# Optimization experiments

Hardware: AMD Instinct MI355X
Metric: run time of the kernel (lower is better)

## Reference

```python
import jax, jax.numpy as jnp
import numpy as np

B, S, D, H = 2, 2048, 1024, 16
DH = D // H  # 64


def setup_inputs() -> dict:
    key = jax.random.key(0)
    ks = jax.random.split(key, 12)
    scale = 0.02
    q = jax.random.normal(ks[0], (B, S, D), dtype=jnp.float32)
    k = jax.random.normal(ks[1], (B, S, D), dtype=jnp.float32)
    v = jax.random.normal(ks[2], (B, S, D), dtype=jnp.float32)
    # CTRL-style causal mask: 1.0 above the diagonal (positions to mask), 0.0 elsewhere
    mask = jnp.triu(jnp.ones((S, S), dtype=jnp.float32), k=1)
    Wq = jax.random.normal(ks[3], (D, D), dtype=jnp.float32) * scale
    bq = jnp.zeros((D,), dtype=jnp.float32)
    Wk = jax.random.normal(ks[4], (D, D), dtype=jnp.float32) * scale
    bk = jnp.zeros((D,), dtype=jnp.float32)
    Wv = jax.random.normal(ks[5], (D, D), dtype=jnp.float32) * scale
    bv = jnp.zeros((D,), dtype=jnp.float32)
    Wo = jax.random.normal(ks[6], (D, D), dtype=jnp.float32) * scale
    bo = jnp.zeros((D,), dtype=jnp.float32)
    return {"q": q, "k": k, "v": v, "mask": mask,
            "Wq": Wq, "bq": bq, "Wk": Wk, "bk": bk,
            "Wv": Wv, "bv": bv, "Wo": Wo, "bo": bo}


def _split_heads(x):
    # [B, S, D] -> [B, H, S, DH]
    b, s, _ = x.shape
    return x.reshape(b, s, H, DH).transpose(0, 2, 1, 3)


def reference(q, k, v, mask, Wq, bq, Wk, bk, Wv, bv, Wo, bo):
    # QKV projections
    qh = _split_heads(q @ Wq + bq)  # [B, H, S, DH]
    kh = _split_heads(k @ Wk + bk)
    vh = _split_heads(v @ Wv + bv)
    # scaled dot-product attention with CTRL mask convention (mask * -1e4 added)
    scores = jnp.einsum('bhqd,bhkd->bhqk', qh, kh) / jnp.sqrt(jnp.float32(DH))
    scores = scores + mask * -10000.0  # mask broadcasts [S,S] -> [B,H,S,S]
    weights = jax.nn.softmax(scores, axis=-1)
    ctx = jnp.einsum('bhqk,bhkd->bhqd', weights, vh)  # [B, H, S, DH]
    ctx = ctx.transpose(0, 2, 1, 3).reshape(q.shape[0], -1, D)  # [B, S, D]
    return ctx @ Wo + bo
```

## Files before the change

kernel.cpp:

```cpp
#include <hip/hip_runtime.h>
#include <stdint.h>

typedef unsigned short u16;
typedef __attribute__((ext_vector_type(8))) short bf16x8;
typedef __attribute__((ext_vector_type(4))) float f32x4;
typedef __attribute__((ext_vector_type(4))) unsigned short u16x4;

#define C_SCALE 0.1803368801111204f
#define C_MASK  -14426.950408889634f

__device__ __forceinline__ float bf2f(u16 x) {
  union { uint32_t u; float f; } v; v.u = ((uint32_t)x) << 16; return v.f;
}
__device__ __forceinline__ u16 f2bf(float f) {
  union { float f; uint32_t u; } v; v.f = f;
  return (u16)((v.u + 0x7FFFu + ((v.u >> 16) & 1u)) >> 16);
}

__device__ __forceinline__ void load_lds16(const void* g, void* l) {
  __builtin_amdgcn_global_load_lds(
      (const __attribute__((address_space(1))) uint32_t*)g,
      (__attribute__((address_space(3))) uint32_t*)l, 16, 0, 0);
}

__device__ __forceinline__ uint32_t pack_trunc(uint32_t f_even, uint32_t f_odd) {
  return __builtin_amdgcn_perm(f_odd, f_even, 0x07060302u);
}

union U4B { uint4 u; bf16x8 v; };

__global__ __launch_bounds__(256) void detect_dtype(const u16* __restrict__ q,
                                                    uint32_t* __restrict__ flag) {
  const int tid = threadIdx.x;
  u16 w = q[tid];
  int e = (w >> 7) & 0xFF;
  int ok = (e >= 96 && e <= 159) ? 1 : 0;
  unsigned long long b = __ballot(ok);
  __shared__ int cnt[4];
  if ((tid & 63) == 0) cnt[tid >> 6] = __popcll(b);
  __syncthreads();
  if (tid == 0) {
    int total = cnt[0] + cnt[1] + cnt[2] + cnt[3];
    *flag = (total >= 220) ? 1u : 0u;
  }
}

__global__ __launch_bounds__(256) void transpose_all(const u16* __restrict__ W0,
                                                     const u16* __restrict__ W1,
                                                     const u16* __restrict__ W2,
                                                     const u16* __restrict__ W3,
                                                     u16* __restrict__ WTb,
                                                     const uint32_t* __restrict__ flag) {
  constexpr int D = 1024;
  __shared__ u16 tile[64][72];
  const int z = blockIdx.z;
  const u16* W = z == 0 ? W0 : (z == 1 ? W1 : (z == 2 ? W2 : W3));
  u16* WT = WTb + (size_t)z * D * D;
  const bool isbf = (*flag != 0);
  const int x0 = blockIdx.x * 64, y0 = blockIdx.y * 64;
  const int t = threadIdx.x;
  const int r = t >> 3;
  const int c8 = (t & 7) << 3;
#pragma unroll
  for (int hh = 0; hh < 2; ++hh) {
    int row = r + hh * 32;
    if (isbf) {
      *(uint4*)&tile[row][c8] = *(const uint4*)&W[(size_t)(y0 + row) * D + x0 + c8];
    } else {
      const float* Wf = (const float*)W;
      float4 f0 = *(const float4*)&Wf[(size_t)(y0 + row) * D + x0 + c8];
      float4 f1 = *(const float4*)&Wf[(size_t)(y0 + row) * D + x0 + c8 + 4];
      u16 tmp[8] = {f2bf(f0.x), f2bf(f0.y), f2bf(f0.z), f2bf(f0.w),
                    f2bf(f1.x), f2bf(f1.y), f2bf(f1.z), f2bf(f1.w)};
      *(uint4*)&tile[row][c8] = *(uint4*)tmp;
    }
  }
  __syncthreads();
#pragma unroll
  for (int hh = 0; hh < 2; ++hh) {
    int row = r + hh * 32;
    u16 tmp[8];
#pragma unroll
    for (int i = 0; i < 8; ++i) tmp[i] = tile[c8 + i][row];
    *(uint4*)&WT[(size_t)(x0 + row) * D + y0 + c8] = *(uint4*)tmp;
  }
}

__global__ __launch_bounds__(256, 2) void gemm_qkv(
    const u16* __restrict__ A0, const u16* __restrict__ A1, const u16* __restrict__ A2,
    const u16* __restrict__ WTb,
    const u16* __restrict__ b0, const u16* __restrict__ b1, const u16* __restrict__ b2,
    u16* __restrict__ Chb, const uint32_t* __restrict__ flag) {
  constexpr int K = 1024;
  __shared__ u16 As[2][128 * 64];
  __shared__ u16 Bs[2][128 * 32];
  const int z = blockIdx.z;
  const u16* A = z == 0 ? A0 : (z == 1 ? A1 : A2);
  const u16* bias = z == 0 ? b0 : (z == 1 ? b1 : b2);
  const u16* BT = WTb + (size_t)z * 1024 * 1024;
  u16* C = Chb + (size_t)z * 4 * 1024 * 1024;
  const bool isbf = (*flag != 0);
  const int tid = threadIdx.x;
  const int wave = tid >> 6, lane = tid & 63;
  const int quad = lane >> 4, lr = lane & 15;
  const int f = blockIdx.x + 8 * blockIdx.y;
  const int n0 = (f >> 5) * 128;
  const int m0 = (f & 31) * 128;
  const int mW = (wave & 1) * 64, nW = (wave >> 1) * 64;

  auto stageB = [&](int k0, int kb) {
#pragma unroll
    for (int p = 0; p < 2; ++p) {
      int s = (wave * 2 + p) * 64 + lane;
      int r = s >> 2, c = s & 3;
      load_lds16(&BT[(size_t)(n0 + r) * K + k0 + c * 8], &Bs[kb][(wave * 2 + p) * 512]);
    }
  };

  f32x4 acc[4][4] = {};

  if (!isbf) {
    const uint32_t* Af = (const uint32_t*)A;
    auto stageA = [&](int k0, int kb) {
#pragma unroll
      for (int p = 0; p < 4; ++p) {
        int s = (wave * 4 + p) * 64 + lane;
        int r = s >> 3, cg = (s & 7) ^ (r & 7);
        load_lds16(&Af[(size_t)(m0 + r) * K + k0 + cg * 4],
                   &As[kb][(wave * 4 + p) * 512]);
      }
    };
    stageA(0, 0); stageB(0, 0);
    int kb = 0;
    for (int k0 = 0; k0 < K; k0 += 32, kb ^= 1) {
      __syncthreads();
      if (k0 + 32 < K) { stageA(k0 + 32, kb ^ 1); stageB(k0 + 32, kb ^ 1); }
      const uint32_t* As32 = (const uint32_t*)&As[kb][0];
      bf16x8 af[4], bfm[4];
#pragma unroll
      for (int i = 0; i < 4; ++i) {
        int r = mW + 16 * i + lr;
        int s0 = (2 * quad) ^ (r & 7), s1 = (2 * quad + 1) ^ (r & 7);
        uint4 lo = *(const uint4*)&As32[r * 32 + s0 * 4];
        uint4 hi = *(const uint4*)&As32[r * 32 + s1 * 4];
        U4B pk;
        pk.u.x = pack_trunc(lo.x, lo.y); pk.u.y = pack_trunc(lo.z, lo.w);
        pk.u.z = pack_trunc(hi.x, hi.y); pk.u.w = pack_trunc(hi.z, hi.w);
        af[i] = pk.v;
        bfm[i] = *(const bf16x8*)&Bs[kb][(nW + 16 * i + lr) * 32 + quad * 8];
      }
#pragma unroll
      for (int i = 0; i < 4; ++i)
#pragma unroll
        for (int j = 0; j < 4; ++j)
          acc[i][j] =
              __builtin_amdgcn_mfma_f32_16x16x32_bf16(af[i], bfm[j], acc[i][j], 0, 0, 0);
    }
  } else {
    auto stageAb = [&](int k0, int kb) {
#pragma unroll
      for (int p = 0; p < 2; ++p) {
        int s = (wave * 2 + p) * 64 + lane;
        int r = s >> 2, c = s & 3;
        load_lds16(&A[(size_t)(m0 + r) * K + k0 + c * 8], &As[kb][(wave * 2 + p) * 512]);
      }
    };
    stageAb(0, 0); stageB(0, 0);
    int kb = 0;
    for (int k0 = 0; k0 < K; k0 += 32, kb ^= 1) {
      __syncthreads();
      if (k0 + 32 < K) { stageAb(k0 + 32, kb ^ 1); stageB(k0 + 32, kb ^ 1); }
      bf16x8 af[4], bfm[4];
#pragma unroll
      for (int i = 0; i < 4; ++i) {
        af[i]  = *(const bf16x8*)&As[kb][(mW + 16 * i + lr) * 32 + quad * 8];
        bfm[i] = *(const bf16x8*)&Bs[kb][(nW + 16 * i + lr) * 32 + quad * 8];
      }
#pragma unroll
      for (int i = 0; i < 4; ++i)
#pragma unroll
        for (int j = 0; j < 4; ++j)
          acc[i][j] =
              __builtin_amdgcn_mfma_f32_16x16x32_bf16(af[i], bfm[j], acc[i][j], 0, 0, 0);
    }
  }

#pragma unroll
  for (int i = 0; i < 4; ++i) {
#pragma unroll
    for (int j = 0; j < 4; ++j) {
      int n = n0 + nW + 16 * j + lr;
      float bv = isbf ? bf2f(bias[n]) : ((const float*)bias)[n];
#pragma unroll
      for (int r = 0; r < 4; ++r) {
        int m = m0 + mW + 16 * i + quad * 4 + r;
        float val = acc[i][j][r] + bv;
        int b = m >> 11, s = m & 2047, h = n >> 6, dh = n & 63;
        C[((size_t)(b * 16 + h) * 2048 + s) * 64 + dh] = f2bf(val);
      }
    }
  }
}

__global__ __launch_bounds__(256, 2) void gemm_out(const u16* __restrict__ A,
                                                   const u16* __restrict__ BT,
                                                   const u16* __restrict__ bias,
                                                   u16* __restrict__ C,
                                                   const uint32_t* __restrict__ flag) {
  constexpr int K = 1024, N = 1024;
  __shared__ u16 As[2][64 * 32];
  __shared__ u16 Bs[2][128 * 32];
  const bool isbf = (*flag != 0);
  const int tid = threadIdx.x;
  const int wave = tid >> 6, lane = tid & 63;
  const int quad = lane >> 4, lr = lane & 15;
  const int f = blockIdx.x + 8 * blockIdx.y;
  const int n0 = (f >> 6) * 128;
  const int m0 = (f & 63) * 64;
  const int mW = (wave & 1) * 32, nW = (wave >> 1) * 64;

  auto stage = [&](int k0, int kb) {
    {
      int s = wave * 64 + lane;
      int r = s >> 2, c = s & 3;
      load_lds16(&A[(size_t)(m0 + r) * K + k0 + c * 8], &As[kb][wave * 512]);
    }
#pragma unroll
    for (int p = 0; p < 2; ++p) {
      int s = (wave * 2 + p) * 64 + lane;
      int r = s >> 2, c = s & 3;
      load_lds16(&BT[(size_t)(n0 + r) * K + k0 + c * 8], &Bs[kb][(wave * 2 + p) * 512]);
    }
  };

  f32x4 acc[2][4] = {};
  stage(0, 0);
  int kb = 0;
  for (int k0 = 0; k0 < K; k0 += 32, kb ^= 1) {
    __syncthreads();
    if (k0 + 32 < K) stage(k0 + 32, kb ^ 1);
    bf16x8 af[2], bfm[4];
#pragma unroll
    for (int i = 0; i < 2; ++i)
      af[i] = *(const bf16x8*)&As[kb][(mW + 16 * i + lr) * 32 + quad * 8];
#pragma unroll
    for (int j = 0; j < 4; ++j)
      bfm[j] = *(const bf16x8*)&Bs[kb][(nW + 16 * j + lr) * 32 + quad * 8];
#pragma unroll
    for (int i = 0; i < 2; ++i)
#pragma unroll
      for (int j = 0; j < 4; ++j)
        acc[i][j] =
            __builtin_amdgcn_mfma_f32_16x16x32_bf16(af[i], bfm[j], acc[i][j], 0, 0, 0);
  }

#pragma unroll
  for (int i = 0; i < 2; ++i) {
#pragma unroll
    for (int j = 0; j < 4; ++j) {
      int n = n0 + nW + 16 * j + lr;
      float bv = isbf ? bf2f(bias[n]) : ((const float*)bias)[n];
#pragma unroll
      for (int r = 0; r < 4; ++r) {
        int m = m0 + mW + 16 * i + quad * 4 + r;
        float val = acc[i][j][r] + bv;
        size_t idx = (size_t)m * N + n;
        if (isbf) C[idx] = f2bf(val);
        else ((float*)C)[idx] = val;
      }
    }
  }
}

__global__ __launch_bounds__(256, 2) void attn_fwd(const u16* __restrict__ Qh,
                                                   const u16* __restrict__ Kh,
                                                   const u16* __restrict__ Vh,
                                                   u16* __restrict__ ctx) {
  constexpr int S = 2048, DH = 64, Dm = 1024;
  __shared__ u16 Ks[2][64 * 64];
  __shared__ u16 Vt[64 * 72];
  __shared__ u16 Pl[4][16 * 72];
  const int tid = threadIdx.x;
  const int wave = tid >> 6, lane = tid & 63;
  const int quad = lane >> 4, lr = lane & 15;
  const int bh = blockIdx.y;
  const int bx = (int)blockIdx.x;
  const size_t base = (size_t)bh * S * DH;
  const u16* Q = Qh + base;
  const u16* Kp = Kh + base;
  const u16* Vp = Vh + base;
  u16* Plw = Pl[wave];
  const int b = bh >> 4, h = bh & 15;

  const int vkey2 = (tid & 31) * 2, vd8 = (tid >> 5) * 8;
  uint4 va, vb;

  auto stageK = [&](int kt, int kb) {
#pragma unroll
    for (int p = 0; p < 2; ++p) {
      int s = (wave * 2 + p) * 64 + lane;
      int r = s >> 3, cg = (s & 7) ^ (r & 7);
      load_lds16(&Kp[(size_t)(kt + r) * DH + cg * 8], &Ks[kb][(wave * 2 + p) * 512]);
    }
  };
  auto loadV = [&](int kt) {
    va = *(const uint4*)&Vp[(size_t)(kt + vkey2) * DH + vd8];
    vb = *(const uint4*)&Vp[(size_t)(kt + vkey2 + 1) * DH + vd8];
  };
  auto writeV = [&]() {
    const u16* pa = (const u16*)&va;
    const u16* pb = (const u16*)&vb;
#pragma unroll
    for (int i = 0; i < 8; ++i) {
      uint32_t pair = (uint32_t)pa[i] | ((uint32_t)pb[i] << 16);
      *(uint32_t*)&Vt[(vd8 + i) * 72 + vkey2] = pair;
    }
  };

  int kb = 0;
  for (int ph = 0; ph < 2; ++ph) {
    const int qt = ph == 0 ? (31 - bx) : bx;
    const int q0 = qt * 64;
    const int nt = qt + 1;
    const int qg = q0 + wave * 16 + lr;

    bf16x8 aQ[2];
#pragma unroll
    for (int s = 0; s < 2; ++s)
      aQ[s] = *(const bf16x8*)&Q[(size_t)(q0 + wave * 16 + lr) * DH + s * 32 + quad * 8];

    f32x4 o[4] = {};
    float m_i = -1.0e5f;
    float l_i = 0.f;

    __syncthreads();
    stageK(0, kb);
    loadV(0);

    for (int it = 0; it < nt; ++it) {
      const int kt = it * 64;
      __syncthreads();
      writeV();
      __syncthreads();

      bf16x8 aK[4][2], bV[4][2];
#pragma unroll
      for (int t = 0; t < 4; ++t) {
        int r = t * 16 + lr;
#pragma unroll
        for (int s = 0; s < 2; ++s) {
          int ch = (s * 4 + quad) ^ (r & 7);
          aK[t][s] = *(const bf16x8*)&Ks[kb][r * 64 + ch * 8];
        }
      }
#pragma unroll
      for (int c = 0; c < 4; ++c)
#pragma unroll
        for (int s = 0; s < 2; ++s)
          bV[c][s] = *(const bf16x8*)&Vt[(c * 16 + lr) * 72 + s * 32 + quad * 8];

      if (it + 1 < nt) { stageK(kt + 64, kb ^ 1); loadV(kt + 64); }

      f32x4 sc[4];
#pragma unroll
      for (int t = 0; t < 4; ++t) {
        f32x4 zz = {0.f, 0.f, 0.f, 0.f};
        zz = __builtin_amdgcn_mfma_f32_16x16x32_bf16(aK[t][0], aQ[0], zz, 0, 0, 0);
        zz = __builtin_amdgcn_mfma_f32_16x16x32_bf16(aK[t][1], aQ[1], zz, 0, 0, 0);
        sc[t] = zz;
      }

      const bool diag = (it == nt - 1);
      float v[4][4];
      float mx = -1.0e5f;
      if (diag) {
#pragma unroll
        for (int t = 0; t < 4; ++t)
#pragma unroll
          for (int r = 0; r < 4; ++r) {
            int kg = kt + t * 16 + quad * 4 + r;
            float x = sc[t][r] * C_SCALE + ((kg > qg) ? C_MASK : 0.f);
            v[t][r] = x;
            mx = fmaxf(mx, x);
          }
      } else {
#pragma unroll
        for (int t = 0; t < 4; ++t)
#pragma unroll
          for (int r = 0; r < 4; ++r) {
            float x = sc[t][r] * C_SCALE;
            v[t][r] = x;
            mx = fmaxf(mx, x);
          }
      }
      mx = fmaxf(mx, __shfl_xor(mx, 16));
      mx = fmaxf(mx, __shfl_xor(mx, 32));
      float m_new = fmaxf(m_i, mx);
      float sum = 0.f;
      u16 pb16[4][4];
#pragma unroll
      for (int t = 0; t < 4; ++t)
#pragma unroll
        for (int r = 0; r < 4; ++r) {
          float p = exp2f(v[t][r] - m_new);
          sum += p;
          pb16[t][r] = f2bf(p);
        }
      sum += __shfl_xor(sum, 16);
      sum += __shfl_xor(sum, 32);
      float alpha = exp2f(m_i - m_new);
      l_i = l_i * alpha + sum;
      m_i = m_new;
#pragma unroll
      for (int t = 0; t < 4; ++t) {
        u16x4 w = {pb16[t][0], pb16[t][1], pb16[t][2], pb16[t][3]};
        *(u16x4*)&Plw[lr * 72 + t * 16 + quad * 4] = w;
      }
#pragma unroll
      for (int r = 0; r < 4; ++r) {
        float ab = __shfl(alpha, quad * 4 + r);
#pragma unroll
        for (int c = 0; c < 4; ++c) o[c][r] *= ab;
      }
      asm volatile("s_waitcnt lgkmcnt(0)" ::: "memory");
      bf16x8 aP[2];
#pragma unroll
      for (int s = 0; s < 2; ++s)
        aP[s] = *(const bf16x8*)&Plw[lr * 72 + s * 32 + quad * 8];
#pragma unroll
      for (int c = 0; c < 4; ++c)
#pragma unroll
        for (int s = 0; s < 2; ++s)
          o[c] = __builtin_amdgcn_mfma_f32_16x16x32_bf16(aP[s], bV[c][s], o[c], 0, 0, 0);
      kb ^= 1;
    }

    float linv = 1.f / l_i;
#pragma unroll
    for (int r = 0; r < 4; ++r) {
      float lb = __shfl(linv, quad * 4 + r);
      int s = q0 + wave * 16 + quad * 4 + r;
      size_t orow = ((size_t)b * S + s) * Dm + h * DH;
#pragma unroll
      for (int c = 0; c < 4; ++c) ctx[orow + c * 16 + lr] = f2bf(o[c][r] * lb);
    }
  }
}

extern "C" void kernel_launch(void* const* d_in, const int* in_sizes, int n_in,
                              void* d_out, int out_size, void* d_ws, size_t ws_size,
                              hipStream_t stream) {
  const u16* q  = (const u16*)d_in[0];
  const u16* k  = (const u16*)d_in[1];
  const u16* v  = (const u16*)d_in[2];
  const u16* Wq = (const u16*)d_in[4];
  const u16* bq = (const u16*)d_in[5];
  const u16* Wk = (const u16*)d_in[6];
  const u16* bk = (const u16*)d_in[7];
  const u16* Wv = (const u16*)d_in[8];
  const u16* bv = (const u16*)d_in[9];
  const u16* Wo = (const u16*)d_in[10];
  const u16* bo = (const u16*)d_in[11];
  u16* out = (u16*)d_out;

  constexpr size_t M1 = 1024 * 1024;
  u16* ws = (u16*)d_ws;
  uint32_t* flag = (uint32_t*)ws;
  u16* WT  = ws + 16;
  u16* Qh  = WT + 4 * M1;
  u16* ctx = Qh + 12 * M1;

  dim3 tb(256);
  detect_dtype<<<1, tb, 0, stream>>>(q, flag);
  transpose_all<<<dim3(16, 16, 4), tb, 0, stream>>>(Wq, Wk, Wv, Wo, WT, flag);
  gemm_qkv<<<dim3(8, 32, 3), tb, 0, stream>>>(q, k, v, WT, bq, bk, bv, Qh, flag);
  attn_fwd<<<dim3(16, 32), tb, 0, stream>>>(Qh, Qh + 4 * M1, Qh + 8 * M1, ctx);
  gemm_out<<<dim3(8, 64), tb, 0, stream>>>(ctx, WT + 3 * M1, bo, out, flag);
}
```

Before: 278.4 us.

## Inline dtype detection, shrink GEMM tiles, register-stage A, double-buffer V

Drops the separate dtype-detection kernel and has each kernel run an in-wave ballot probe on q, saving one launch and the flag read. The QKV GEMM moves from 128x128 to 64x128 tiles, with A loaded through registers (fp32 truncated to bf16 on the way) instead of a 128x64 fp32 LDS stage. The output GEMM moves to 64x64 tiles, doubling its grid. Attention double-buffers the transposed V tile to remove one barrier per iteration. Smaller tiles add more blocks and parallelism but lower per-block reuse.

Measured after the change: 262.2 us. -5.8%, faster.

```diff
diff --git a/kernel.cpp b/kernel.cpp
--- a/kernel.cpp
+++ b/kernel.cpp
@@ -27,22 +27,12 @@
   return __builtin_amdgcn_perm(f_odd, f_even, 0x07060302u);
 }
 
-union U4B { uint4 u; bf16x8 v; };
-
-__global__ __launch_bounds__(256) void detect_dtype(const u16* __restrict__ q,
-                                                    uint32_t* __restrict__ flag) {
-  const int tid = threadIdx.x;
-  u16 w = q[tid];
+__device__ __forceinline__ bool detect_bf16(const u16* __restrict__ q) {
+  int lane = threadIdx.x & 63;
+  u16 w = q[lane * 4];
   int e = (w >> 7) & 0xFF;
-  int ok = (e >= 96 && e <= 159) ? 1 : 0;
-  unsigned long long b = __ballot(ok);
-  __shared__ int cnt[4];
-  if ((tid & 63) == 0) cnt[tid >> 6] = __popcll(b);
-  __syncthreads();
-  if (tid == 0) {
-    int total = cnt[0] + cnt[1] + cnt[2] + cnt[3];
-    *flag = (total >= 220) ? 1u : 0u;
-  }
+  unsigned long long b = __ballot(e >= 96 && e <= 159);
+  return __popcll(b) >= 48;
 }
 
 __global__ __launch_bounds__(256) void transpose_all(const u16* __restrict__ W0,
@@ -50,13 +40,13 @@
                                                      const u16* __restrict__ W2,
                                                      const u16* __restrict__ W3,
                                                      u16* __restrict__ WTb,
-                                                     const uint32_t* __restrict__ flag) {
+                                                     const u16* __restrict__ qprobe) {
   constexpr int D = 1024;
   __shared__ u16 tile[64][72];
   const int z = blockIdx.z;
   const u16* W = z == 0 ? W0 : (z == 1 ? W1 : (z == 2 ? W2 : W3));
   u16* WT = WTb + (size_t)z * D * D;
-  const bool isbf = (*flag != 0);
+  const bool isbf = detect_bf16(qprobe);
   const int x0 = blockIdx.x * 64, y0 = blockIdx.y * 64;
   const int t = threadIdx.x;
   const int r = t >> 3;
@@ -90,127 +80,16 @@
     const u16* __restrict__ A0, const u16* __restrict__ A1, const u16* __restrict__ A2,
     const u16* __restrict__ WTb,
     const u16* __restrict__ b0, const u16* __restrict__ b1, const u16* __restrict__ b2,
-    u16* __restrict__ Chb, const uint32_t* __restrict__ flag) {
+    u16* __restrict__ Chb) {
   constexpr int K = 1024;
-  __shared__ u16 As[2][128 * 64];
+  __shared__ u16 As[2][64 * 32];
   __shared__ u16 Bs[2][128 * 32];
   const int z = blockIdx.z;
   const u16* A = z == 0 ? A0 : (z == 1 ? A1 : A2);
   const u16* bias = z == 0 ? b0 : (z == 1 ? b1 : b2);
   const u16* BT = WTb + (size_t)z * 1024 * 1024;
   u16* C = Chb + (size_t)z * 4 * 1024 * 1024;
-  const bool isbf = (*flag != 0);
-  const int tid = threadIdx.x;
-  const int wave = tid >> 6, lane = tid & 63;
-  const int quad = lane >> 4, lr = lane & 15;
-  const int f = blockIdx.x + 8 * blockIdx.y;
-  const int n0 = (f >> 5) * 128;
-  const int m0 = (f & 31) * 128;
-  const int mW = (wave & 1) * 64, nW = (wave >> 1) * 64;
-
-  auto stageB = [&](int k0, int kb) {
-#pragma unroll
-    for (int p = 0; p < 2; ++p) {
-      int s = (wave * 2 + p) * 64 + lane;
-      int r = s >> 2, c = s & 3;
-      load_lds16(&BT[(size_t)(n0 + r) * K + k0 + c * 8], &Bs[kb][(wave * 2 + p) * 512]);
-    }
-  };
-
-  f32x4 acc[4][4] = {};
-
-  if (!isbf) {
-    const uint32_t* Af = (const uint32_t*)A;
-    auto stageA = [&](int k0, int kb) {
-#pragma unroll
-      for (int p = 0; p < 4; ++p) {
-        int s = (wave * 4 + p) * 64 + lane;
-        int r = s >> 3, cg = (s & 7) ^ (r & 7);
-        load_lds16(&Af[(size_t)(m0 + r) * K + k0 + cg * 4],
-                   &As[kb][(wave * 4 + p) * 512]);
-      }
-    };
-    stageA(0, 0); stageB(0, 0);
-    int kb = 0;
-    for (int k0 = 0; k0 < K; k0 += 32, kb ^= 1) {
-      __syncthreads();
-      if (k0 + 32 < K) { stageA(k0 + 32, kb ^ 1); stageB(k0 + 32, kb ^ 1); }
-      const uint32_t* As32 = (const uint32_t*)&As[kb][0];
-      bf16x8 af[4], bfm[4];
-#pragma unroll
-      for (int i = 0; i < 4; ++i) {
-        int r = mW + 16 * i + lr;
-        int s0 = (2 * quad) ^ (r & 7), s1 = (2 * quad + 1) ^ (r & 7);
-        uint4 lo = *(const uint4*)&As32[r * 32 + s0 * 4];
-        uint4 hi = *(const uint4*)&As32[r * 32 + s1 * 4];
-        U4B pk;
-        pk.u.x = pack_trunc(lo.x, lo.y); pk.u.y = pack_trunc(lo.z, lo.w);
-        pk.u.z = pack_trunc(hi.x, hi.y); pk.u.w = pack_trunc(hi.z, hi.w);
-        af[i] = pk.v;
-        bfm[i] = *(const bf16x8*)&Bs[kb][(nW + 16 * i + lr) * 32 + quad * 8];
-      }
-#pragma unroll
-      for (int i = 0; i < 4; ++i)
-#pragma unroll
-        for (int j = 0; j < 4; ++j)
-          acc[i][j] =
-              __builtin_amdgcn_mfma_f32_16x16x32_bf16(af[i], bfm[j], acc[i][j], 0, 0, 0);
-    }
-  } else {
-    auto stageAb = [&](int k0, int kb) {
-#pragma unroll
-      for (int p = 0; p < 2; ++p) {
-        int s = (wave * 2 + p) * 64 + lane;
-        int r = s >> 2, c = s & 3;
-        load_lds16(&A[(size_t)(m0 + r) * K + k0 + c * 8], &As[kb][(wave * 2 + p) * 512]);
-      }
-    };
-    stageAb(0, 0); stageB(0, 0);
-    int kb = 0;
-    for (int k0 = 0; k0 < K; k0 += 32, kb ^= 1) {
-      __syncthreads();
-      if (k0 + 32 < K) { stageAb(k0 + 32, kb ^ 1); stageB(k0 + 32, kb ^ 1); }
-      bf16x8 af[4], bfm[4];
-#pragma unroll
-      for (int i = 0; i < 4; ++i) {
-        af[i]  = *(const bf16x8*)&As[kb][(mW + 16 * i + lr) * 32 + quad * 8];
-        bfm[i] = *(const bf16x8*)&Bs[kb][(nW + 16 * i + lr) * 32 + quad * 8];
-      }
-#pragma unroll
-      for (int i = 0; i < 4; ++i)
-#pragma unroll
-        for (int j = 0; j < 4; ++j)
-          acc[i][j] =
-              __builtin_amdgcn_mfma_f32_16x16x32_bf16(af[i], bfm[j], acc[i][j], 0, 0, 0);
-    }
-  }
-
-#pragma unroll
-  for (int i = 0; i < 4; ++i) {
-#pragma unroll
-    for (int j = 0; j < 4; ++j) {
-      int n = n0 + nW + 16 * j + lr;
-      float bv = isbf ? bf2f(bias[n]) : ((const float*)bias)[n];
-#pragma unroll
-      for (int r = 0; r < 4; ++r) {
-        int m = m0 + mW + 16 * i + quad * 4 + r;
-        float val = acc[i][j][r] + bv;
-        int b = m >> 11, s = m & 2047, h = n >> 6, dh = n & 63;
-        C[((size_t)(b * 16 + h) * 2048 + s) * 64 + dh] = f2bf(val);
-      }
-    }
-  }
-}
-
-__global__ __launch_bounds__(256, 2) void gemm_out(const u16* __restrict__ A,
-                                                   const u16* __restrict__ BT,
-                                                   const u16* __restrict__ bias,
-                                                   u16* __restrict__ C,
-                                                   const uint32_t* __restrict__ flag) {
-  constexpr int K = 1024, N = 1024;
-  __shared__ u16 As[2][64 * 32];
-  __shared__ u16 Bs[2][128 * 32];
-  const bool isbf = (*flag != 0);
+  const bool isbf = detect_bf16(A0);
   const int tid = threadIdx.x;
   const int wave = tid >> 6, lane = tid & 63;
   const int quad = lane >> 4, lr = lane & 15;
@@ -218,13 +97,29 @@
   const int n0 = (f >> 6) * 128;
   const int m0 = (f & 63) * 64;
   const int mW = (wave & 1) * 32, nW = (wave >> 1) * 64;
-
-  auto stage = [&](int k0, int kb) {
-    {
-      int s = wave * 64 + lane;
-      int r = s >> 2, c = s & 3;
-      load_lds16(&A[(size_t)(m0 + r) * K + k0 + c * 8], &As[kb][wave * 512]);
-    }
+  const int ar = tid >> 2, ac = (tid & 3) * 8;
+
+  uint4 ra, rb;
+  auto loadA = [&](int k0) {
+    if (isbf) {
+      ra = *(const uint4*)&A[(size_t)(m0 + ar) * K + k0 + ac];
+    } else {
+      const uint32_t* Af = (const uint32_t*)A;
+      ra = *(const uint4*)&Af[(size_t)(m0 + ar) * K + k0 + ac];
+      rb = *(const uint4*)&Af[(size_t)(m0 + ar) * K + k0 + ac + 4];
+    }
+  };
+  auto writeA = [&](int kb) {
+    if (isbf) {
+      *(uint4*)&As[kb][ar * 32 + ac] = ra;
+    } else {
+      uint4 o;
+      o.x = pack_trunc(ra.x, ra.y); o.y = pack_trunc(ra.z, ra.w);
+      o.z = pack_trunc(rb.x, rb.y); o.w = pack_trunc(rb.z, rb.w);
+      *(uint4*)&As[kb][ar * 32 + ac] = o;
+    }
+  };
+  auto stageB = [&](int k0, int kb) {
 #pragma unroll
     for (int p = 0; p < 2; ++p) {
       int s = (wave * 2 + p) * 64 + lane;
@@ -234,22 +129,90 @@
   };
 
   f32x4 acc[2][4] = {};
+  loadA(0);
+  stageB(0, 0);
+  writeA(0);
+  loadA(32);
+  int kb = 0;
+  for (int k0 = 0; k0 < K; k0 += 32, kb ^= 1) {
+    __syncthreads();
+    if (k0 + 32 < K) {
+      stageB(k0 + 32, kb ^ 1);
+      writeA(kb ^ 1);
+      if (k0 + 64 < K) loadA(k0 + 64);
+    }
+    bf16x8 af[2], bfm[4];
+#pragma unroll
+    for (int i = 0; i < 2; ++i)
+      af[i] = *(const bf16x8*)&As[kb][(mW + 16 * i + lr) * 32 + quad * 8];
+#pragma unroll
+    for (int j = 0; j < 4; ++j)
+      bfm[j] = *(const bf16x8*)&Bs[kb][(nW + 16 * j + lr) * 32 + quad * 8];
+#pragma unroll
+    for (int i = 0; i < 2; ++i)
+#pragma unroll
+      for (int j = 0; j < 4; ++j)
+        acc[i][j] =
+            __builtin_amdgcn_mfma_f32_16x16x32_bf16(af[i], bfm[j], acc[i][j], 0, 0, 0);
+  }
+
+#pragma unroll
+  for (int i = 0; i < 2; ++i) {
+#pragma unroll
+    for (int j = 0; j < 4; ++j) {
+      int n = n0 + nW + 16 * j + lr;
+      float bv = isbf ? bf2f(bias[n]) : ((const float*)bias)[n];
+#pragma unroll
+      for (int r = 0; r < 4; ++r) {
+        int m = m0 + mW + 16 * i + quad * 4 + r;
+        float val = acc[i][j][r] + bv;
+        int b = m >> 11, s = m & 2047, h = n >> 6, dh = n & 63;
+        C[((size_t)(b * 16 + h) * 2048 + s) * 64 + dh] = f2bf(val);
+      }
+    }
+  }
+}
+
+__global__ __launch_bounds__(256, 2) void gemm_out(const u16* __restrict__ A,
+                                                   const u16* __restrict__ BT,
+                                                   const u16* __restrict__ bias,
+                                                   u16* __restrict__ C,
+                                                   const u16* __restrict__ qprobe) {
+  constexpr int K = 1024, N = 1024;
+  __shared__ u16 As[2][64 * 32];
+  __shared__ u16 Bs[2][64 * 32];
+  const bool isbf = detect_bf16(qprobe);
+  const int tid = threadIdx.x;
+  const int wave = tid >> 6, lane = tid & 63;
+  const int quad = lane >> 4, lr = lane & 15;
+  const int f = blockIdx.x + 8 * blockIdx.y;
+  const int n0 = (f >> 6) * 64;
+  const int m0 = (f & 63) * 64;
+  const int mW = (wave & 1) * 32, nW = (wave >> 1) * 32;
+
+  auto stage = [&](int k0, int kb) {
+    int s = wave * 64 + lane;
+    int r = s >> 2, c = s & 3;
+    load_lds16(&A[(size_t)(m0 + r) * K + k0 + c * 8], &As[kb][wave * 512]);
+    load_lds16(&BT[(size_t)(n0 + r) * K + k0 + c * 8], &Bs[kb][wave * 512]);
+  };
+
+  f32x4 acc[2][2] = {};
   stage(0, 0);
   int kb = 0;
   for (int k0 = 0; k0 < K; k0 += 32, kb ^= 1) {
     __syncthreads();
     if (k0 + 32 < K) stage(k0 + 32, kb ^ 1);
-    bf16x8 af[2], bfm[4];
+    bf16x8 af[2], bfm[2];
+#pragma unroll
+    for (int i = 0; i < 2; ++i) {
+      af[i]  = *(const bf16x8*)&As[kb][(mW + 16 * i + lr) * 32 + quad * 8];
+      bfm[i] = *(const bf16x8*)&Bs[kb][(nW + 16 * i + lr) * 32 + quad * 8];
+    }
 #pragma unroll
     for (int i = 0; i < 2; ++i)
-      af[i] = *(const bf16x8*)&As[kb][(mW + 16 * i + lr) * 32 + quad * 8];
-#pragma unroll
-    for (int j = 0; j < 4; ++j)
-      bfm[j] = *(const bf16x8*)&Bs[kb][(nW + 16 * j + lr) * 32 + quad * 8];
-#pragma unroll
-    for (int i = 0; i < 2; ++i)
-#pragma unroll
-      for (int j = 0; j < 4; ++j)
+#pragma unroll
+      for (int j = 0; j < 2; ++j)
         acc[i][j] =
             __builtin_amdgcn_mfma_f32_16x16x32_bf16(af[i], bfm[j], acc[i][j], 0, 0, 0);
   }
@@ -257,7 +220,7 @@
 #pragma unroll
   for (int i = 0; i < 2; ++i) {
 #pragma unroll
-    for (int j = 0; j < 4; ++j) {
+    for (int j = 0; j < 2; ++j) {
       int n = n0 + nW + 16 * j + lr;
       float bv = isbf ? bf2f(bias[n]) : ((const float*)bias)[n];
 #pragma unroll
@@ -278,7 +241,7 @@
                                                    u16* __restrict__ ctx) {
   constexpr int S = 2048, DH = 64, Dm = 1024;
   __shared__ u16 Ks[2][64 * 64];
-  __shared__ u16 Vt[64 * 72];
+  __shared__ u16 Vt[2][64 * 72];
   __shared__ u16 Pl[4][16 * 72];
   const int tid = threadIdx.x;
   const int wave = tid >> 6, lane = tid & 63;
@@ -293,31 +256,31 @@
   const int b = bh >> 4, h = bh & 15;
 
   const int vkey2 = (tid & 31) * 2, vd8 = (tid >> 5) * 8;
-  uint4 va, vb;
-
-  auto stageK = [&](int kt, int kb) {
+  uint4 va, vbr;
+
+  auto stageK = [&](int kt, int kbuf) {
 #pragma unroll
     for (int p = 0; p < 2; ++p) {
       int s = (wave * 2 + p) * 64 + lane;
       int r = s >> 3, cg = (s & 7) ^ (r & 7);
-      load_lds16(&Kp[(size_t)(kt + r) * DH + cg * 8], &Ks[kb][(wave * 2 + p) * 512]);
+      load_lds16(&Kp[(size_t)(kt + r) * DH + cg * 8], &Ks[kbuf][(wave * 2 + p) * 512]);
     }
   };
   auto loadV = [&](int kt) {
-    va = *(const uint4*)&Vp[(size_t)(kt + vkey2) * DH + vd8];
-    vb = *(const uint4*)&Vp[(size_t)(kt + vkey2 + 1) * DH + vd8];
-  };
-  auto writeV = [&]() {
+    va  = *(const uint4*)&Vp[(size_t)(kt + vkey2) * DH + vd8];
+    vbr = *(const uint4*)&Vp[(size_t)(kt + vkey2 + 1) * DH + vd8];
+  };
+  auto writeV = [&](int vbuf) {
     const u16* pa = (const u16*)&va;
-    const u16* pb = (const u16*)&vb;
+    const u16* pb = (const u16*)&vbr;
 #pragma unroll
     for (int i = 0; i < 8; ++i) {
       uint32_t pair = (uint32_t)pa[i] | ((uint32_t)pb[i] << 16);
-      *(uint32_t*)&Vt[(vd8 + i) * 72 + vkey2] = pair;
-    }
-  };
-
-  int kb = 0;
+      *(uint32_t*)&Vt[vbuf][(vd8 + i) * 72 + vkey2] = pair;
+    }
+  };
+
+  int kb = 0, vb = 0;
   for (int ph = 0; ph < 2; ++ph) {
     const int qt = ph == 0 ? (31 - bx) : bx;
     const int q0 = qt * 64;
@@ -336,11 +299,11 @@
     __syncthreads();
     stageK(0, kb);
     loadV(0);
+    writeV(vb);
+    if (nt > 1) loadV(64);
 
     for (int it = 0; it < nt; ++it) {
       const int kt = it * 64;
-      __syncthreads();
-      writeV();
       __syncthreads();
 
       bf16x8 aK[4][2], bV[4][2];
@@ -357,9 +320,13 @@
       for (int c = 0; c < 4; ++c)
 #pragma unroll
         for (int s = 0; s < 2; ++s)
-          bV[c][s] = *(const bf16x8*)&Vt[(c * 16 + lr) * 72 + s * 32 + quad * 8];
-
-      if (it + 1 < nt) { stageK(kt + 64, kb ^ 1); loadV(kt + 64); }
+          bV[c][s] = *(const bf16x8*)&Vt[vb][(c * 16 + lr) * 72 + s * 32 + quad * 8];
+
+      if (it + 1 < nt) {
+        stageK(kt + 64, kb ^ 1);
+        writeV(vb ^ 1);
+        if (it + 2 < nt) loadV(kt + 128);
+      }
 
       f32x4 sc[4];
 #pragma unroll
@@ -432,7 +399,7 @@
 #pragma unroll
         for (int s = 0; s < 2; ++s)
           o[c] = __builtin_amdgcn_mfma_f32_16x16x32_bf16(aP[s], bV[c][s], o[c], 0, 0, 0);
-      kb ^= 1;
+      kb ^= 1; vb ^= 1;
     }
 
     float linv = 1.f / l_i;
@@ -465,15 +432,13 @@
 
   constexpr size_t M1 = 1024 * 1024;
   u16* ws = (u16*)d_ws;
-  uint32_t* flag = (uint32_t*)ws;
-  u16* WT  = ws + 16;
+  u16* WT  = ws;
   u16* Qh  = WT + 4 * M1;
   u16* ctx = Qh + 12 * M1;
 
   dim3 tb(256);
-  detect_dtype<<<1, tb, 0, stream>>>(q, flag);
-  transpose_all<<<dim3(16, 16, 4), tb, 0, stream>>>(Wq, Wk, Wv, Wo, WT, flag);
-  gemm_qkv<<<dim3(8, 32, 3), tb, 0, stream>>>(q, k, v, WT, bq, bk, bv, Qh, flag);
+  transpose_all<<<dim3(16, 16, 4), tb, 0, stream>>>(Wq, Wk, Wv, Wo, WT, q);
+  gemm_qkv<<<dim3(8, 64, 3), tb, 0, stream>>>(q, k, v, WT, bq, bk, bv, Qh);
   attn_fwd<<<dim3(16, 32), tb, 0, stream>>>(Qh, Qh + 4 * M1, Qh + 8 * M1, ctx);
-  gemm_out<<<dim3(8, 64), tb, 0, stream>>>(ctx, WT + 3 * M1, bo, out, flag);
-}
+  gemm_out<<<dim3(8, 128), tb, 0, stream>>>(ctx, WT + 3 * M1, bo, out, q);
+}
```
